# Kernel tuning notes

Hardware: AMD Instinct MI355X
Metric: run time of the kernel (lower is better)

The kernel has to match this reference:

```python
import jax, jax.numpy as jnp
import numpy as np

N_NODES = 100000
N_EDGES = 3200000
NEG_SLOPE = 0.2  # PyG GATConv default


def _gat_conv(x, src, dst, W, a_src, a_dst, b, num_nodes):
    # x: [N, Fin]; src/dst: [E'] (self-loops already appended)
    h = x @ W                                   # [N, Fout]
    alpha_src = h @ a_src                       # [N]
    alpha_dst = h @ a_dst                       # [N]
    e = jax.nn.leaky_relu(alpha_src[src] + alpha_dst[dst], NEG_SLOPE)  # [E']
    # segment softmax over incoming edges of each destination node
    e_max = jax.ops.segment_max(e, dst, num_segments=num_nodes)
    e_exp = jnp.exp(e - e_max[dst])
    denom = jax.ops.segment_sum(e_exp, dst, num_segments=num_nodes)
    alpha = e_exp / (denom[dst] + 1e-16)        # [E']
    out = jax.ops.segment_sum(h[src] * alpha[:, None], dst, num_segments=num_nodes)
    return out + b


def setup_inputs() -> dict:
    key = jax.random.key(0)
    ks = jax.random.split(key, 10)
    x = jax.random.normal(ks[0], (N_NODES, 1), jnp.float32)
    edge_index = jax.random.randint(ks[1], (2, N_EDGES), 0, N_NODES, dtype=jnp.int64)
    s1 = 1.0  # glorot-ish scales
    return {
        "x": x,
        "edge_index": edge_index,
        "W1": jax.random.normal(ks[2], (1, 20), jnp.float32) * s1,
        "a_src1": jax.random.normal(ks[3], (20,), jnp.float32) * 0.3,
        "a_dst1": jax.random.normal(ks[4], (20,), jnp.float32) * 0.3,
        "b1": jnp.zeros((20,), jnp.float32),
        "W2": jax.random.normal(ks[5], (20, 20), jnp.float32) * (1.0 / np.sqrt(20.0)),
        "a_src2": jax.random.normal(ks[6], (20,), jnp.float32) * 0.3,
        "a_dst2": jax.random.normal(ks[7], (20,), jnp.float32) * 0.3,
        "b2": jnp.zeros((20,), jnp.float32),
        "Wl": jax.random.normal(ks[8], (20, 1), jnp.float32) * (1.0 / np.sqrt(20.0)),
        "bl": jnp.zeros((1,), jnp.float32),
    }


def reference(x, edge_index, W1, a_src1, a_dst1, b1, W2, a_src2, a_dst2, b2, Wl, bl):
    n = x.shape[0]
    loop = jnp.arange(n, dtype=edge_index.dtype)
    src = jnp.concatenate([edge_index[0], loop])  # add_self_loops=True
    dst = jnp.concatenate([edge_index[1], loop])
    h = _gat_conv(x, src, dst, W1, a_src1, a_dst1, b1, n)
    h = jax.nn.relu(h)
    h = _gat_conv(h, src, dst, W2, a_src2, a_dst2, b2, n)
    h = jax.nn.relu(h)
    return h @ Wl + bl  # [N, 1]
```

## Files before the change

### kernel.cpp

```cpp
#include <hip/hip_runtime.h>
#include <hip/hip_fp16.h>

#define FDIM 20
#define NSLOPE 0.2f
#define BSHIFT 7
#define BSIZE 128
#define BCAP 4800
#define MAXBUCK 800
#define PGRID 512
#define HSTRIDE 32
#define ABLK 512
#define ITMAX 7
#define CHCAP 6272
#define OFFSTRIDE 132

__device__ __forceinline__ float lrelu(float v) { return v > 0.f ? v : NSLOPE * v; }

__global__ void __launch_bounds__(1024)
k_part(const int* __restrict__ ei, int E, int nbuck,
       const float* __restrict__ x, const float* __restrict__ W1,
       const float* __restrict__ a_src, const float* __restrict__ a_dst,
       float2* __restrict__ PX, float* __restrict__ AD,
       int* __restrict__ gcur, int* __restrict__ slab, int N)
{
    __shared__ int hist[MAXBUCK];
    __shared__ int lofs[MAXBUCK];
    __shared__ int gbase[MAXBUCK];
    __shared__ int sbuf[CHCAP];
    __shared__ unsigned short sbk[CHCAP];
    const int tid = threadIdx.x;

    {
        int g = blockIdx.x * 1024 + tid;
        if (g < N) {
            float cs = 0.f, cd = 0.f;
#pragma unroll
            for (int f = 0; f < FDIM; ++f) {
                float w = W1[f]; cs += w * a_src[f]; cd += w * a_dst[f];
            }
            float xv = x[g];
            PX[g] = make_float2(xv * cs, xv);
            AD[g] = xv * cd;
        }
    }

    const int chunk = (E + PGRID - 1) / PGRID;
    const int c0 = blockIdx.x * chunk;
    const int c1 = min(c0 + chunk, E);
    for (int t = tid; t < nbuck; t += 1024) hist[t] = 0;
    __syncthreads();

    int ent[ITMAX], meta[ITMAX];
#pragma unroll
    for (int it = 0; it < ITMAX; ++it) {
        int i = c0 + tid + (it << 10);
        meta[it] = -1;
        if (i < c1) {
            int s = ei[i], d = ei[E + i];
            int b = d >> BSHIFT;
            int lp = atomicAdd(&hist[b], 1);
            ent[it]  = (s << BSHIFT) | (d & (BSIZE - 1));
            meta[it] = (lp << 10) | b;
        }
    }
    __syncthreads();

    int myc = 0;
    if (tid < nbuck) {
        myc = hist[tid];
        lofs[tid] = myc;
        gbase[tid] = myc ? atomicAdd(gcur + tid, myc) : 0;
    }
    __syncthreads();
    for (int o = 1; o < nbuck; o <<= 1) {
        int v = 0;
        if (tid < nbuck && tid >= o) v = lofs[tid - o];
        __syncthreads();
        if (tid < nbuck && tid >= o) lofs[tid] += v;
        __syncthreads();
    }
    if (tid < nbuck) lofs[tid] -= myc;
    __syncthreads();

#pragma unroll
    for (int it = 0; it < ITMAX; ++it) {
        int m = meta[it];
        if (m >= 0) {
            int b  = m & 1023;
            int lp = m >> 10;
            int pos = lofs[b] + lp;
            sbuf[pos] = ent[it];
            sbk[pos]  = (unsigned short)b;
        }
    }
    __syncthreads();

    const int cnt = c1 - c0;
    for (int i = tid; i < cnt; i += 1024) {
        int b  = sbk[i];
        int gp = gbase[b] + (i - lofs[b]);
        if (gp < BCAP) slab[(size_t)b * BCAP + gp] = sbuf[i];
    }
}

__device__ __forceinline__ void sort_bucket(const int* __restrict__ sp, int cnt,
                                            int* __restrict__ sedge,
                                            int* __restrict__ off,
                                            int* __restrict__ cur)
{
    const int tid = threadIdx.x;
    if (tid < BSIZE + 1) off[tid] = 0;
    __syncthreads();
    for (int i = tid; i < cnt; i += ABLK)
        atomicAdd(&off[(sp[i] & (BSIZE - 1)) + 1], 1);
    __syncthreads();
    if (tid < 64) {
        int a = off[2 * tid + 1];
        int c = off[2 * tid + 2];
        int s = a + c;
#pragma unroll
        for (int o = 1; o < 64; o <<= 1) {
            int t = __shfl_up(s, o);
            if (tid >= o) s += t;
        }
        int ex = s - a - c;
        off[2 * tid]     = ex;
        off[2 * tid + 1] = ex + a;
        cur[2 * tid]     = ex;
        cur[2 * tid + 1] = ex + a;
        if (tid == 63) off[BSIZE] = s;
    }
    __syncthreads();
    for (int i = tid; i < cnt; i += ABLK) {
        int e = sp[i];
        int pos = atomicAdd(&cur[e & (BSIZE - 1)], 1);
        sedge[pos] = e >> BSHIFT;
    }
    __syncthreads();
}

__global__ void __launch_bounds__(ABLK)
k_agg1(const int* __restrict__ gcur, const int* __restrict__ slab,
       const float2* __restrict__ PX, const float* __restrict__ AD,
       const float* __restrict__ W1, const float* __restrict__ b1,
       const float* __restrict__ W2,
       const float* __restrict__ as2w, const float* __restrict__ ad2w,
       __half* __restrict__ H, float* __restrict__ AD2,
       int* __restrict__ sedge_g, int* __restrict__ off_g, int N)
{
    __shared__ int sedge[BCAP];
    __shared__ int off[BSIZE + 1], cur[BSIZE];
    __shared__ float sAD[BSIZE];
    __shared__ float sW1[FDIM], sb1[FDIM], sW2[FDIM * FDIM], sas[FDIM], sad[FDIM];
    const int tid = threadIdx.x;
    const int b = blockIdx.x;
    const int dbase = b << BSHIFT;
    if (tid < BSIZE) { int d = dbase + tid; sAD[tid] = (d < N) ? AD[d] : 0.f; }
    for (int t = tid; t < FDIM * FDIM; t += ABLK) sW2[t] = W2[t];
    if (tid >= 480 && tid < 480 + FDIM) {
        int k = tid - 480;
        sW1[k] = W1[k]; sb1[k] = b1[k]; sas[k] = as2w[k]; sad[k] = ad2w[k];
    }
    const int cnt = min(gcur[b], BCAP);
    sort_bucket(slab + (size_t)b * BCAP, cnt, sedge, off, cur);

    for (int i = tid; i < cnt; i += ABLK) sedge_g[(size_t)b * BCAP + i] = sedge[i];
    if (tid <= BSIZE) off_g[b * OFFSTRIDE + tid] = off[tid];

    const int dl = tid >> 2, sub = tid & 3;
    const float adv = sAD[dl];
    float den = 0.f, sx = 0.f;
    const int e1 = off[dl + 1];
#pragma unroll 4
    for (int j = off[dl] + sub; j < e1; j += 4) {
        int s = sedge[j];
        float2 p = PX[s];
        float w = __expf(lrelu(p.x + adv));
        den += w; sx += w * p.y;
    }
    den += __shfl_xor(den, 1); den += __shfl_xor(den, 2);
    sx  += __shfl_xor(sx, 1);  sx  += __shfl_xor(sx, 2);
    const int d = dbase + dl;
    if (d < N) {
        float2 p = PX[d];
        float w = __expf(lrelu(p.x + adv));
        den += w; sx += w * p.y;
        float sv = sx / (den + 1e-16f);
        float tk[FDIM];
#pragma unroll
        for (int k = 0; k < FDIM; ++k) {
            float tv = sv * sW1[k] + sb1[k];
            tk[k] = tv > 0.f ? tv : 0.f;
        }
        const int fbase = sub << 3;
        const int nf = (sub < 2) ? 8 : (sub == 2 ? 4 : 0);
        float hv[8];
        float pas = 0.f, pad = 0.f;
#pragma unroll
        for (int t = 0; t < 8; ++t) {
            float hsum = 0.f;
            if (t < nf) {
#pragma unroll
                for (int k = 0; k < FDIM; ++k)
                    hsum += tk[k] * sW2[k * FDIM + fbase + t];
                pas += hsum * sas[fbase + t];
                pad += hsum * sad[fbase + t];
            }
            hv[t] = hsum;
        }
        pas += __shfl_xor(pas, 1); pas += __shfl_xor(pas, 2);
        pad += __shfl_xor(pad, 1); pad += __shfl_xor(pad, 2);
        __half2 p01 = __halves2half2(__float2half(hv[0]), __float2half(hv[1]));
        __half2 p23 = __halves2half2(__float2half(hv[2]), __float2half(hv[3]));
        __half2 p45 = __halves2half2(__float2half(hv[4]), __float2half(hv[5]));
        __half2 p67 = __halves2half2(__float2half(hv[6]), __float2half(hv[7]));
        uint4 q;
        q.x = *(unsigned*)&p01; q.y = *(unsigned*)&p23;
        q.z = *(unsigned*)&p45; q.w = *(unsigned*)&p67;
        if (sub == 2) { q.z = __float_as_uint(pas); q.w = 0u; }
        if (sub < 3) ((uint4*)(H + (size_t)d * HSTRIDE))[sub] = q;
        else AD2[d] = pad;
    }
}

__global__ void __launch_bounds__(ABLK)
k_agg2(const int* __restrict__ gcur, const int* __restrict__ sedge_g,
       const int* __restrict__ off_g,
       const __half* __restrict__ H, const float* __restrict__ AD2,
       const float* __restrict__ b2, const float* __restrict__ Wl,
       const float* __restrict__ bl,
       float* __restrict__ out, int N)
{
    __shared__ int sedge[BCAP];
    __shared__ int off[BSIZE + 1];
    __shared__ float sAD[BSIZE];
    __shared__ float sb2[FDIM], sWl[FDIM];
    const int tid = threadIdx.x;
    const int b = blockIdx.x;
    const int dbase = b << BSHIFT;
    if (tid < BSIZE) { int d = dbase + tid; sAD[tid] = (d < N) ? AD2[d] : 0.f; }
    if (tid >= 480 && tid < 480 + FDIM) {
        int k = tid - 480;
        sb2[k] = b2[k]; sWl[k] = Wl[k];
    }
    const int cnt = min(gcur[b], BCAP);
    for (int i = tid; i < cnt; i += ABLK) sedge[i] = sedge_g[(size_t)b * BCAP + i];
    if (tid <= BSIZE) off[tid] = off_g[b * OFFSTRIDE + tid];
    __syncthreads();

    const int dl = tid >> 2, sub = tid & 3;
    const float adv = sAD[dl];
    float den = 0.f;
    float acc[FDIM];
#pragma unroll
    for (int k = 0; k < FDIM; ++k) acc[k] = 0.f;
    const int e1 = off[dl + 1];
#pragma unroll 4
    for (int j = off[dl] + sub; j < e1; j += 4) {
        int s = sedge[j];
        const uint4* rp = (const uint4*)(H + (size_t)s * HSTRIDE);
        uint4 a = rp[0];
        uint4 bb = rp[1];
        uint4 c = rp[2];
        float w = __expf(lrelu(__uint_as_float(c.z) + adv));
        den += w;
        float2 f;
        f = __half22float2(*(__half2*)&a.x);  acc[0]  += w * f.x; acc[1]  += w * f.y;
        f = __half22float2(*(__half2*)&a.y);  acc[2]  += w * f.x; acc[3]  += w * f.y;
        f = __half22float2(*(__half2*)&a.z);  acc[4]  += w * f.x; acc[5]  += w * f.y;
        f = __half22float2(*(__half2*)&a.w);  acc[6]  += w * f.x; acc[7]  += w * f.y;
        f = __half22float2(*(__half2*)&bb.x); acc[8]  += w * f.x; acc[9]  += w * f.y;
        f = __half22float2(*(__half2*)&bb.y); acc[10] += w * f.x; acc[11] += w * f.y;
        f = __half22float2(*(__half2*)&bb.z); acc[12] += w * f.x; acc[13] += w * f.y;
        f = __half22float2(*(__half2*)&bb.w); acc[14] += w * f.x; acc[15] += w * f.y;
        f = __half22float2(*(__half2*)&c.x);  acc[16] += w * f.x; acc[17] += w * f.y;
        f = __half22float2(*(__half2*)&c.y);  acc[18] += w * f.x; acc[19] += w * f.y;
    }
    den += __shfl_xor(den, 1); den += __shfl_xor(den, 2);
#pragma unroll
    for (int k = 0; k < FDIM; ++k) {
        acc[k] += __shfl_xor(acc[k], 1);
        acc[k] += __shfl_xor(acc[k], 2);
    }
    const int d = dbase + dl;
    if (sub == 0 && d < N) {
        const uint4* rp = (const uint4*)(H + (size_t)d * HSTRIDE);
        uint4 a = rp[0], bb = rp[1], c = rp[2];
        float w = __expf(lrelu(__uint_as_float(c.z) + adv));
        den += w;
        float hv[FDIM];
        float2 f;
        f = __half22float2(*(__half2*)&a.x);  hv[0]  = f.x; hv[1]  = f.y;
        f = __half22float2(*(__half2*)&a.y);  hv[2]  = f.x; hv[3]  = f.y;
        f = __half22float2(*(__half2*)&a.z);  hv[4]  = f.x; hv[5]  = f.y;
        f = __half22float2(*(__half2*)&a.w);  hv[6]  = f.x; hv[7]  = f.y;
        f = __half22float2(*(__half2*)&bb.x); hv[8]  = f.x; hv[9]  = f.y;
        f = __half22float2(*(__half2*)&bb.y); hv[10] = f.x; hv[11] = f.y;
        f = __half22float2(*(__half2*)&bb.z); hv[12] = f.x; hv[13] = f.y;
        f = __half22float2(*(__half2*)&bb.w); hv[14] = f.x; hv[15] = f.y;
        f = __half22float2(*(__half2*)&c.x);  hv[16] = f.x; hv[17] = f.y;
        f = __half22float2(*(__half2*)&c.y);  hv[18] = f.x; hv[19] = f.y;
        float inv = 1.f / (den + 1e-16f);
        float r = 0.f;
#pragma unroll
        for (int k = 0; k < FDIM; ++k) {
            float v = (acc[k] + w * hv[k]) * inv + sb2[k];
            v = v > 0.f ? v : 0.f;
            r += v * sWl[k];
        }
        out[d] = r + bl[0];
    }
}

extern "C" void kernel_launch(void* const* d_in, const int* in_sizes, int n_in,
                              void* d_out, int out_size, void* d_ws, size_t ws_size,
                              hipStream_t stream)
{
    const float* x      = (const float*)d_in[0];
    const int*   ei     = (const int*)d_in[1];
    const float* W1     = (const float*)d_in[2];
    const float* a_src1 = (const float*)d_in[3];
    const float* a_dst1 = (const float*)d_in[4];
    const float* b1     = (const float*)d_in[5];
    const float* W2     = (const float*)d_in[6];
    const float* a_src2 = (const float*)d_in[7];
    const float* a_dst2 = (const float*)d_in[8];
    const float* b2     = (const float*)d_in[9];
    const float* Wl     = (const float*)d_in[10];
    const float* bl     = (const float*)d_in[11];
    float* out = (float*)d_out;

    const int N = in_sizes[0];
    const int E = in_sizes[1] / 2;
    const int NBUCK = (N + BSIZE - 1) >> BSHIFT;

    __half* H    = (__half*)d_ws;
    float2* PX   = (float2*)(H + (size_t)N * HSTRIDE);
    float*  AD   = (float*)(PX + N);
    float*  AD2  = AD + N;
    int*  gcur   = (int*)(AD2 + N);
    int*  slab   = gcur + MAXBUCK;
    int*  sedge_g = slab + (size_t)MAXBUCK * BCAP;
    int*  off_g   = sedge_g + (size_t)MAXBUCK * BCAP;

    hipMemsetAsync(gcur, 0, MAXBUCK * sizeof(int), stream);
    k_part<<<PGRID, 1024, 0, stream>>>(ei, E, NBUCK, x, W1, a_src1, a_dst1,
                                       PX, AD, gcur, slab, N);
    k_agg1<<<NBUCK, ABLK, 0, stream>>>(gcur, slab, PX, AD, W1, b1, W2,
                                       a_src2, a_dst2, H, AD2, sedge_g, off_g, N);
    k_agg2<<<NBUCK, ABLK, 0, stream>>>(gcur, sedge_g, off_g, H, AD2, b2, Wl, bl, out, N);
}
```

Measured before the change: 176.6 us.

## Use persistent work-queue blocks for aggregation and a wavefront-shuffle bucket scan

Both aggregation kernels now run a fixed grid of persistent blocks. Each block repeatedly claims the next destination bucket through a global atomic counter instead of mapping one block to one bucket. Separately, the per-block prefix sum over bucket counts in the partition kernel is replaced by a two-level wavefront shuffle scan, removing the log-step shared-memory loop and its barriers. The queue aims to smooth load imbalance from uneven bucket sizes and cut scan latency, at the cost of an extra atomic and barrier per bucket. With the grid close to the bucket count, few blocks process more than one bucket.

```diff
diff --git a/kernel.cpp b/kernel.cpp
--- a/kernel.cpp
+++ b/kernel.cpp
@@ -10,6 +10,7 @@
 #define PGRID 512
 #define HSTRIDE 32
 #define ABLK 512
+#define AGRID 768
 #define ITMAX 7
 #define CHCAP 6272
 #define OFFSTRIDE 132
@@ -28,6 +29,7 @@
     __shared__ int gbase[MAXBUCK];
     __shared__ int sbuf[CHCAP];
     __shared__ unsigned short sbk[CHCAP];
+    __shared__ int wsum[16];
     const int tid = threadIdx.x;
 
     {
@@ -68,18 +70,28 @@
     int myc = 0;
     if (tid < nbuck) {
         myc = hist[tid];
-        lofs[tid] = myc;
         gbase[tid] = myc ? atomicAdd(gcur + tid, myc) : 0;
     }
-    __syncthreads();
-    for (int o = 1; o < nbuck; o <<= 1) {
-        int v = 0;
-        if (tid < nbuck && tid >= o) v = lofs[tid - o];
-        __syncthreads();
-        if (tid < nbuck && tid >= o) lofs[tid] += v;
-        __syncthreads();
-    }
-    if (tid < nbuck) lofs[tid] -= myc;
+    int inc = myc;
+#pragma unroll
+    for (int o = 1; o < 64; o <<= 1) {
+        int t = __shfl_up(inc, o);
+        if ((tid & 63) >= o) inc += t;
+    }
+    if ((tid & 63) == 63) wsum[tid >> 6] = inc;
+    __syncthreads();
+    if (tid < 16) {
+        int v = wsum[tid];
+        int e = v;
+#pragma unroll
+        for (int o = 1; o < 16; o <<= 1) {
+            int t = __shfl_up(e, o);
+            if (tid >= o) e += t;
+        }
+        wsum[tid] = e - v;
+    }
+    __syncthreads();
+    if (tid < nbuck) lofs[tid] = inc - myc + wsum[tid >> 6];
     __syncthreads();
 
 #pragma unroll
@@ -146,80 +158,89 @@
        const float* __restrict__ W2,
        const float* __restrict__ as2w, const float* __restrict__ ad2w,
        __half* __restrict__ H, float* __restrict__ AD2,
-       int* __restrict__ sedge_g, int* __restrict__ off_g, int N)
+       int* __restrict__ sedge_g, int* __restrict__ off_g,
+       int* __restrict__ qhead, int N, int nbuck)
 {
     __shared__ int sedge[BCAP];
     __shared__ int off[BSIZE + 1], cur[BSIZE];
     __shared__ float sAD[BSIZE];
     __shared__ float sW1[FDIM], sb1[FDIM], sW2[FDIM * FDIM], sas[FDIM], sad[FDIM];
+    __shared__ int curb;
     const int tid = threadIdx.x;
-    const int b = blockIdx.x;
-    const int dbase = b << BSHIFT;
-    if (tid < BSIZE) { int d = dbase + tid; sAD[tid] = (d < N) ? AD[d] : 0.f; }
+
     for (int t = tid; t < FDIM * FDIM; t += ABLK) sW2[t] = W2[t];
     if (tid >= 480 && tid < 480 + FDIM) {
         int k = tid - 480;
         sW1[k] = W1[k]; sb1[k] = b1[k]; sas[k] = as2w[k]; sad[k] = ad2w[k];
     }
-    const int cnt = min(gcur[b], BCAP);
-    sort_bucket(slab + (size_t)b * BCAP, cnt, sedge, off, cur);
-
-    for (int i = tid; i < cnt; i += ABLK) sedge_g[(size_t)b * BCAP + i] = sedge[i];
-    if (tid <= BSIZE) off_g[b * OFFSTRIDE + tid] = off[tid];
-
-    const int dl = tid >> 2, sub = tid & 3;
-    const float adv = sAD[dl];
-    float den = 0.f, sx = 0.f;
-    const int e1 = off[dl + 1];
+
+    for (;;) {
+        if (tid == 0) curb = atomicAdd(qhead, 1);
+        __syncthreads();
+        const int b = curb;
+        if (b >= nbuck) break;
+        const int dbase = b << BSHIFT;
+        if (tid < BSIZE) { int d = dbase + tid; sAD[tid] = (d < N) ? AD[d] : 0.f; }
+        const int cnt = min(gcur[b], BCAP);
+        sort_bucket(slab + (size_t)b * BCAP, cnt, sedge, off, cur);
+
+        for (int i = tid; i < cnt; i += ABLK) sedge_g[(size_t)b * BCAP + i] = sedge[i];
+        if (tid <= BSIZE) off_g[b * OFFSTRIDE + tid] = off[tid];
+
+        const int dl = tid >> 2, sub = tid & 3;
+        const float adv = sAD[dl];
+        float den = 0.f, sx = 0.f;
+        const int e1 = off[dl + 1];
 #pragma unroll 4
-    for (int j = off[dl] + sub; j < e1; j += 4) {
-        int s = sedge[j];
-        float2 p = PX[s];
-        float w = __expf(lrelu(p.x + adv));
-        den += w; sx += w * p.y;
-    }
-    den += __shfl_xor(den, 1); den += __shfl_xor(den, 2);
-    sx  += __shfl_xor(sx, 1);  sx  += __shfl_xor(sx, 2);
-    const int d = dbase + dl;
-    if (d < N) {
-        float2 p = PX[d];
-        float w = __expf(lrelu(p.x + adv));
-        den += w; sx += w * p.y;
-        float sv = sx / (den + 1e-16f);
-        float tk[FDIM];
-#pragma unroll
-        for (int k = 0; k < FDIM; ++k) {
-            float tv = sv * sW1[k] + sb1[k];
-            tk[k] = tv > 0.f ? tv : 0.f;
-        }
-        const int fbase = sub << 3;
-        const int nf = (sub < 2) ? 8 : (sub == 2 ? 4 : 0);
-        float hv[8];
-        float pas = 0.f, pad = 0.f;
-#pragma unroll
-        for (int t = 0; t < 8; ++t) {
-            float hsum = 0.f;
-            if (t < nf) {
-#pragma unroll
-                for (int k = 0; k < FDIM; ++k)
-                    hsum += tk[k] * sW2[k * FDIM + fbase + t];
-                pas += hsum * sas[fbase + t];
-                pad += hsum * sad[fbase + t];
+        for (int j = off[dl] + sub; j < e1; j += 4) {
+            int s = sedge[j];
+            float2 p = PX[s];
+            float w = __expf(lrelu(p.x + adv));
+            den += w; sx += w * p.y;
+        }
+        den += __shfl_xor(den, 1); den += __shfl_xor(den, 2);
+        sx  += __shfl_xor(sx, 1);  sx  += __shfl_xor(sx, 2);
+        const int d = dbase + dl;
+        if (d < N) {
+            float2 p = PX[d];
+            float w = __expf(lrelu(p.x + adv));
+            den += w; sx += w * p.y;
+            float sv = sx / (den + 1e-16f);
+            float tk[FDIM];
+#pragma unroll
+            for (int k = 0; k < FDIM; ++k) {
+                float tv = sv * sW1[k] + sb1[k];
+                tk[k] = tv > 0.f ? tv : 0.f;
             }
-            hv[t] = hsum;
-        }
-        pas += __shfl_xor(pas, 1); pas += __shfl_xor(pas, 2);
-        pad += __shfl_xor(pad, 1); pad += __shfl_xor(pad, 2);
-        __half2 p01 = __halves2half2(__float2half(hv[0]), __float2half(hv[1]));
-        __half2 p23 = __halves2half2(__float2half(hv[2]), __float2half(hv[3]));
-        __half2 p45 = __halves2half2(__float2half(hv[4]), __float2half(hv[5]));
-        __half2 p67 = __halves2half2(__float2half(hv[6]), __float2half(hv[7]));
-        uint4 q;
-        q.x = *(unsigned*)&p01; q.y = *(unsigned*)&p23;
-        q.z = *(unsigned*)&p45; q.w = *(unsigned*)&p67;
-        if (sub == 2) { q.z = __float_as_uint(pas); q.w = 0u; }
-        if (sub < 3) ((uint4*)(H + (size_t)d * HSTRIDE))[sub] = q;
-        else AD2[d] = pad;
+            const int fbase = sub << 3;
+            const int nf = (sub < 2) ? 8 : (sub == 2 ? 4 : 0);
+            float hv[8];
+            float pas = 0.f, pad = 0.f;
+#pragma unroll
+            for (int t = 0; t < 8; ++t) {
+                float hsum = 0.f;
+                if (t < nf) {
+#pragma unroll
+                    for (int k = 0; k < FDIM; ++k)
+                        hsum += tk[k] * sW2[k * FDIM + fbase + t];
+                    pas += hsum * sas[fbase + t];
+                    pad += hsum * sad[fbase + t];
+                }
+                hv[t] = hsum;
+            }
+            pas += __shfl_xor(pas, 1); pas += __shfl_xor(pas, 2);
+            pad += __shfl_xor(pad, 1); pad += __shfl_xor(pad, 2);
+            __half2 p01 = __halves2half2(__float2half(hv[0]), __float2half(hv[1]));
+            __half2 p23 = __halves2half2(__float2half(hv[2]), __float2half(hv[3]));
+            __half2 p45 = __halves2half2(__float2half(hv[4]), __float2half(hv[5]));
+            __half2 p67 = __halves2half2(__float2half(hv[6]), __float2half(hv[7]));
+            uint4 q;
+            q.x = *(unsigned*)&p01; q.y = *(unsigned*)&p23;
+            q.z = *(unsigned*)&p45; q.w = *(unsigned*)&p67;
+            if (sub == 2) { q.z = __float_as_uint(pas); q.w = 0u; }
+            if (sub < 3) ((uint4*)(H + (size_t)d * HSTRIDE))[sub] = q;
+            else AD2[d] = pad;
+        }
     }
 }
 
@@ -229,86 +250,94 @@
        const __half* __restrict__ H, const float* __restrict__ AD2,
        const float* __restrict__ b2, const float* __restrict__ Wl,
        const float* __restrict__ bl,
-       float* __restrict__ out, int N)
+       float* __restrict__ out, int* __restrict__ qhead, int N, int nbuck)
 {
     __shared__ int sedge[BCAP];
     __shared__ int off[BSIZE + 1];
     __shared__ float sAD[BSIZE];
     __shared__ float sb2[FDIM], sWl[FDIM];
+    __shared__ int curb;
     const int tid = threadIdx.x;
-    const int b = blockIdx.x;
-    const int dbase = b << BSHIFT;
-    if (tid < BSIZE) { int d = dbase + tid; sAD[tid] = (d < N) ? AD2[d] : 0.f; }
+
     if (tid >= 480 && tid < 480 + FDIM) {
         int k = tid - 480;
         sb2[k] = b2[k]; sWl[k] = Wl[k];
     }
-    const int cnt = min(gcur[b], BCAP);
-    for (int i = tid; i < cnt; i += ABLK) sedge[i] = sedge_g[(size_t)b * BCAP + i];
-    if (tid <= BSIZE) off[tid] = off_g[b * OFFSTRIDE + tid];
-    __syncthreads();
-
-    const int dl = tid >> 2, sub = tid & 3;
-    const float adv = sAD[dl];
-    float den = 0.f;
-    float acc[FDIM];
-#pragma unroll
-    for (int k = 0; k < FDIM; ++k) acc[k] = 0.f;
-    const int e1 = off[dl + 1];
+
+    for (;;) {
+        if (tid == 0) curb = atomicAdd(qhead, 1);
+        __syncthreads();
+        const int b = curb;
+        if (b >= nbuck) break;
+        const int dbase = b << BSHIFT;
+        if (tid < BSIZE) { int d = dbase + tid; sAD[tid] = (d < N) ? AD2[d] : 0.f; }
+        const int cnt = min(gcur[b], BCAP);
+        for (int i = tid; i < cnt; i += ABLK) sedge[i] = sedge_g[(size_t)b * BCAP + i];
+        if (tid <= BSIZE) off[tid] = off_g[b * OFFSTRIDE + tid];
+        __syncthreads();
+
+        const int dl = tid >> 2, sub = tid & 3;
+        const float adv = sAD[dl];
+        float den = 0.f;
+        float acc[FDIM];
+#pragma unroll
+        for (int k = 0; k < FDIM; ++k) acc[k] = 0.f;
+        const int e1 = off[dl + 1];
 #pragma unroll 4
-    for (int j = off[dl] + sub; j < e1; j += 4) {
-        int s = sedge[j];
-        const uint4* rp = (const uint4*)(H + (size_t)s * HSTRIDE);
-        uint4 a = rp[0];
-        uint4 bb = rp[1];
-        uint4 c = rp[2];
-        float w = __expf(lrelu(__uint_as_float(c.z) + adv));
-        den += w;
-        float2 f;
-        f = __half22float2(*(__half2*)&a.x);  acc[0]  += w * f.x; acc[1]  += w * f.y;
-        f = __half22float2(*(__half2*)&a.y);  acc[2]  += w * f.x; acc[3]  += w * f.y;
-        f = __half22float2(*(__half2*)&a.z);  acc[4]  += w * f.x; acc[5]  += w * f.y;
-        f = __half22float2(*(__half2*)&a.w);  acc[6]  += w * f.x; acc[7]  += w * f.y;
-        f = __half22float2(*(__half2*)&bb.x); acc[8]  += w * f.x; acc[9]  += w * f.y;
-        f = __half22float2(*(__half2*)&bb.y); acc[10] += w * f.x; acc[11] += w * f.y;
-        f = __half22float2(*(__half2*)&bb.z); acc[12] += w * f.x; acc[13] += w * f.y;
-        f = __half22float2(*(__half2*)&bb.w); acc[14] += w * f.x; acc[15] += w * f.y;
-        f = __half22float2(*(__half2*)&c.x);  acc[16] += w * f.x; acc[17] += w * f.y;
-        f = __half22float2(*(__half2*)&c.y);  acc[18] += w * f.x; acc[19] += w * f.y;
-    }
-    den += __shfl_xor(den, 1); den += __shfl_xor(den, 2);
-#pragma unroll
-    for (int k = 0; k < FDIM; ++k) {
-        acc[k] += __shfl_xor(acc[k], 1);
-        acc[k] += __shfl_xor(acc[k], 2);
-    }
-    const int d = dbase + dl;
-    if (sub == 0 && d < N) {
-        const uint4* rp = (const uint4*)(H + (size_t)d * HSTRIDE);
-        uint4 a = rp[0], bb = rp[1], c = rp[2];
-        float w = __expf(lrelu(__uint_as_float(c.z) + adv));
-        den += w;
-        float hv[FDIM];
-        float2 f;
-        f = __half22float2(*(__half2*)&a.x);  hv[0]  = f.x; hv[1]  = f.y;
-        f = __half22float2(*(__half2*)&a.y);  hv[2]  = f.x; hv[3]  = f.y;
-        f = __half22float2(*(__half2*)&a.z);  hv[4]  = f.x; hv[5]  = f.y;
-        f = __half22float2(*(__half2*)&a.w);  hv[6]  = f.x; hv[7]  = f.y;
-        f = __half22float2(*(__half2*)&bb.x); hv[8]  = f.x; hv[9]  = f.y;
-        f = __half22float2(*(__half2*)&bb.y); hv[10] = f.x; hv[11] = f.y;
-        f = __half22float2(*(__half2*)&bb.z); hv[12] = f.x; hv[13] = f.y;
-        f = __half22float2(*(__half2*)&bb.w); hv[14] = f.x; hv[15] = f.y;
-        f = __half22float2(*(__half2*)&c.x);  hv[16] = f.x; hv[17] = f.y;
-        f = __half22float2(*(__half2*)&c.y);  hv[18] = f.x; hv[19] = f.y;
-        float inv = 1.f / (den + 1e-16f);
-        float r = 0.f;
+        for (int j = off[dl] + sub; j < e1; j += 4) {
+            int s = sedge[j];
+            const uint4* rp = (const uint4*)(H + (size_t)s * HSTRIDE);
+            uint4 a = rp[0];
+            uint4 bb = rp[1];
+            uint4 c = rp[2];
+            float w = __expf(lrelu(__uint_as_float(c.z) + adv));
+            den += w;
+            float2 f;
+            f = __half22float2(*(__half2*)&a.x);  acc[0]  += w * f.x; acc[1]  += w * f.y;
+            f = __half22float2(*(__half2*)&a.y);  acc[2]  += w * f.x; acc[3]  += w * f.y;
+            f = __half22float2(*(__half2*)&a.z);  acc[4]  += w * f.x; acc[5]  += w * f.y;
+            f = __half22float2(*(__half2*)&a.w);  acc[6]  += w * f.x; acc[7]  += w * f.y;
+            f = __half22float2(*(__half2*)&bb.x); acc[8]  += w * f.x; acc[9]  += w * f.y;
+            f = __half22float2(*(__half2*)&bb.y); acc[10] += w * f.x; acc[11] += w * f.y;
+            f = __half22float2(*(__half2*)&bb.z); acc[12] += w * f.x; acc[13] += w * f.y;
+            f = __half22float2(*(__half2*)&bb.w); acc[14] += w * f.x; acc[15] += w * f.y;
+            f = __half22float2(*(__half2*)&c.x);  acc[16] += w * f.x; acc[17] += w * f.y;
+            f = __half22float2(*(__half2*)&c.y);  acc[18] += w * f.x; acc[19] += w * f.y;
+        }
+        den += __shfl_xor(den, 1); den += __shfl_xor(den, 2);
 #pragma unroll
         for (int k = 0; k < FDIM; ++k) {
-            float v = (acc[k] + w * hv[k]) * inv + sb2[k];
-            v = v > 0.f ? v : 0.f;
-            r += v * sWl[k];
-        }
-        out[d] = r + bl[0];
+            acc[k] += __shfl_xor(acc[k], 1);
+            acc[k] += __shfl_xor(acc[k], 2);
+        }
+        const int d = dbase + dl;
+        if (sub == 0 && d < N) {
+            const uint4* rp = (const uint4*)(H + (size_t)d * HSTRIDE);
+            uint4 a = rp[0], bb = rp[1], c = rp[2];
+            float w = __expf(lrelu(__uint_as_float(c.z) + adv));
+            den += w;
+            float hv[FDIM];
+            float2 f;
+            f = __half22float2(*(__half2*)&a.x);  hv[0]  = f.x; hv[1]  = f.y;
+            f = __half22float2(*(__half2*)&a.y);  hv[2]  = f.x; hv[3]  = f.y;
+            f = __half22float2(*(__half2*)&a.z);  hv[4]  = f.x; hv[5]  = f.y;
+            f = __half22float2(*(__half2*)&a.w);  hv[6]  = f.x; hv[7]  = f.y;
+            f = __half22float2(*(__half2*)&bb.x); hv[8]  = f.x; hv[9]  = f.y;
+            f = __half22float2(*(__half2*)&bb.y); hv[10] = f.x; hv[11] = f.y;
+            f = __half22float2(*(__half2*)&bb.z); hv[12] = f.x; hv[13] = f.y;
+            f = __half22float2(*(__half2*)&bb.w); hv[14] = f.x; hv[15] = f.y;
+            f = __half22float2(*(__half2*)&c.x);  hv[16] = f.x; hv[17] = f.y;
+            f = __half22float2(*(__half2*)&c.y);  hv[18] = f.x; hv[19] = f.y;
+            float inv = 1.f / (den + 1e-16f);
+            float r = 0.f;
+#pragma unroll
+            for (int k = 0; k < FDIM; ++k) {
+                float v = (acc[k] + w * hv[k]) * inv + sb2[k];
+                v = v > 0.f ? v : 0.f;
+                r += v * sWl[k];
+            }
+            out[d] = r + bl[0];
+        }
     }
 }
 
@@ -339,14 +368,17 @@
     float*  AD   = (float*)(PX + N);
     float*  AD2  = AD + N;
     int*  gcur   = (int*)(AD2 + N);
-    int*  slab   = gcur + MAXBUCK;
+    int*  qh     = gcur + MAXBUCK;
+    int*  slab   = gcur + MAXBUCK + 2;
     int*  sedge_g = slab + (size_t)MAXBUCK * BCAP;
     int*  off_g   = sedge_g + (size_t)MAXBUCK * BCAP;
 
-    hipMemsetAsync(gcur, 0, MAXBUCK * sizeof(int), stream);
+    hipMemsetAsync(gcur, 0, (MAXBUCK + 2) * sizeof(int), stream);
     k_part<<<PGRID, 1024, 0, stream>>>(ei, E, NBUCK, x, W1, a_src1, a_dst1,
                                        PX, AD, gcur, slab, N);
-    k_agg1<<<NBUCK, ABLK, 0, stream>>>(gcur, slab, PX, AD, W1, b1, W2,
-                                       a_src2, a_dst2, H, AD2, sedge_g, off_g, N);
-    k_agg2<<<NBUCK, ABLK, 0, stream>>>(gcur, sedge_g, off_g, H, AD2, b2, Wl, bl, out, N);
-}
+    k_agg1<<<AGRID, ABLK, 0, stream>>>(gcur, slab, PX, AD, W1, b1, W2,
+                                       a_src2, a_dst2, H, AD2, sedge_g, off_g,
+                                       qh, N, NBUCK);
+    k_agg2<<<AGRID, ABLK, 0, stream>>>(gcur, sedge_g, off_g, H, AD2, b2, Wl, bl,
+                                       out, qh + 1, N, NBUCK);
+}
```

Result: slower. 195.5 us (+10.7%).
